# Kernel optimization log

Measured on AMD Instinct MI355X. Metric: run time of the kernel, lower is better.

The kernel has to match this reference:

```python
import jax, jax.numpy as jnp
import numpy as np

SOFT_CAP = 20.0
NEG_BIG = -1e9


def setup_inputs() -> dict:
    key = jax.random.key(0)
    kq, kk, kv = jax.random.split(key, 3)
    T, H, D = 3072, 16, 128
    lens = np.array([1024, 768, 640, 640], dtype=np.int32)  # sums to T, max 1024
    cu = np.concatenate([[0], np.cumsum(lens)]).astype(np.int32)
    q = jax.random.normal(kq, (T, H, D), dtype=jnp.float32)
    k = jax.random.normal(kk, (T, H, D), dtype=jnp.float32)
    v = jax.random.normal(kv, (T, H, D), dtype=jnp.float32)
    return {
        "q": q, "k": k, "v": v,
        "cu_seqlens_q": jnp.asarray(cu), "cu_seqlens_k": jnp.asarray(cu),
        "max_seqlen_q": 1024, "max_seqlen_k": 1024,
    }


def _varlen_attention(q, k, v, cu_q, cu_k, S_q, S_k):
    # q,k,v: [T, H, D] packed; cu_*: [B+1] prefix sums; S_*: static max seqlens
    T, H, D = q.shape
    B = cu_q.shape[0] - 1
    lens_q = cu_q[1:] - cu_q[:-1]  # [B]
    lens_k = cu_k[1:] - cu_k[:-1]
    ar_q = jnp.arange(S_q)
    ar_k = jnp.arange(S_k)
    # pad packed tokens into [B, S, H, D]
    idx_q = jnp.clip(cu_q[:-1, None] + ar_q[None, :], 0, T - 1)  # [B, S_q]
    idx_k = jnp.clip(cu_k[:-1, None] + ar_k[None, :], 0, k.shape[0] - 1)
    mask_k = ar_k[None, :] < lens_k[:, None]  # [B, S_k] valid keys
    qp = q[idx_q]  # [B, S_q, H, D]
    kp = k[idx_k]  # [B, S_k, H, D]
    vp = v[idx_k]
    scale = 1.0 / jnp.sqrt(jnp.float32(D))
    scores = jnp.einsum("bqhd,bkhd->bhqk", qp, kp) * scale  # [B, H, S_q, S_k] fp32
    scores = jnp.tanh(scores / SOFT_CAP) * SOFT_CAP  # logit soft-cap
    scores = jnp.where(mask_k[:, None, None, :], scores, NEG_BIG)
    w = jax.nn.softmax(scores, axis=-1)
    out = jnp.einsum("bhqk,bkhd->bqhd", w, vp)  # [B, S_q, H, D]
    # unpad back to packed [T, H, D]
    t = jnp.arange(T)
    seg = jnp.searchsorted(cu_q, t, side="right") - 1  # sequence id per token
    pos = seg * S_q + (t - cu_q[seg])
    return out.reshape(B * S_q, H, D)[pos]


def reference(q, k, v, cu_seqlens_q, cu_seqlens_k, max_seqlen_q, max_seqlen_k):
    return _varlen_attention(q, k, v, cu_seqlens_q, cu_seqlens_k,
                             int(max_seqlen_q), int(max_seqlen_k))
```

## Files before the change

### kernel.cpp

```cpp
#include <hip/hip_runtime.h>

#define H_ 16
#define D_ 128

typedef __attribute__((ext_vector_type(4))) float f32x4;
typedef __attribute__((ext_vector_type(8))) short bf8_t;
typedef __attribute__((ext_vector_type(4))) unsigned int u32x4;

__device__ __forceinline__ unsigned cvt_pk(float a, float b) {
  unsigned r;
  asm("v_cvt_pk_bf16_f32 %0, %1, %2" : "=v"(r) : "v"(a), "v"(b));
  return r;
}

__device__ __forceinline__ float exp2a(float x) {
  float r;
  asm("v_exp_f32 %0, %1" : "=v"(r) : "v"(x));
  return r;
}

__device__ __forceinline__ bf8_t cvt8(const f32x4 a, const f32x4 b) {
  u32x4 r;
  r[0] = cvt_pk(a[0], a[1]); r[1] = cvt_pk(a[2], a[3]);
  r[2] = cvt_pk(b[0], b[1]); r[3] = cvt_pk(b[2], b[3]);
  return __builtin_bit_cast(bf8_t, r);
}

__global__ __launch_bounds__(128)
void conv_kv(const float* __restrict__ K, const float* __restrict__ V,
             const int* __restrict__ cuk, short* __restrict__ Kbf,
             short* __restrict__ Vt, int B, int T) {
  const int J0 = blockIdx.x * 8;
  const int h  = blockIdx.y;
  int b = 0;
  while (b + 1 < B && J0 >= cuk[b + 1]) ++b;
  const int k0 = cuk[b];

  {
    const int g = J0 + (threadIdx.x >> 4);
    const int c = threadIdx.x & 15;
    const int sub = c ^ ((g - k0) & 7);
    const float* src = K + ((size_t)g * H_ + h) * D_ + sub * 8;
    *(bf8_t*)(Kbf + ((size_t)g * H_ + h) * D_ + c * 8) =
        cvt8(*(const f32x4*)src, *(const f32x4*)(src + 4));
  }
  {
    const int d  = threadIdx.x;
    const int j0 = J0 - k0;
    const int base = k0 + (j0 >> 6) * 64 + 32 * ((j0 >> 5) & 1) + 4 * ((j0 >> 3) & 3);
    float v[8];
    #pragma unroll
    for (int s = 0; s < 8; ++s)
      v[s] = V[((size_t)(base + 16 * (s >> 2) + (s & 3)) * H_ + h) * D_ + d];
    u32x4 w;
    w[0] = cvt_pk(v[0], v[1]); w[1] = cvt_pk(v[2], v[3]);
    w[2] = cvt_pk(v[4], v[5]); w[3] = cvt_pk(v[6], v[7]);
    *(u32x4*)(Vt + ((size_t)h * D_ + d) * T + J0) = w;
  }
}

__global__ __launch_bounds__(256, 2)
void fa_main(const float* __restrict__ Q, const short* __restrict__ Kbf,
             const short* __restrict__ Vt, const int* __restrict__ cuq,
             const int* __restrict__ cuk, float* __restrict__ O, int B, int T) {
  __shared__ __align__(16) short k_lds[2][64 * 128];
  __shared__ __align__(16) short v_lds[2][64 * 128];

  const int slot = blockIdx.x;
  int bmax = 0, nmax = 0, tot = 0;
  for (int bb = 0; bb < B; ++bb) {
    const int nk = (cuk[bb + 1] - cuk[bb] + 63) >> 6;
    if (nk > nmax) { nmax = nk; bmax = bb; }
    tot += ((cuq[bb + 1] - cuq[bb] + 127) >> 7) * 16;
  }
  if (slot >= tot) return;
  const int L = ((cuq[bmax + 1] - cuq[bmax] + 127) >> 7) * 16;
  const int halfS = (tot - L) >> 1;

  int b = -1, item = 0;
  if (slot >= halfS && slot < halfS + L) {
    b = bmax; item = slot - halfS;
  } else {
    int sidx = (slot < halfS) ? slot : slot - L;
    for (int bb = 0; bb < B; ++bb) {
      if (bb == bmax) continue;
      const int it = ((cuq[bb + 1] - cuq[bb] + 127) >> 7) * 16;
      if (sidx < it) { b = bb; item = sidx; break; }
      sidx -= it;
    }
    if (b < 0) return;
  }
  const int qt = item >> 4;
  const int h  = item & 15;

  const int q0   = cuq[b];
  const int lenq = cuq[b + 1] - q0;
  const int k0   = cuk[b];
  const int lenk = cuk[b + 1] - k0;
  const int nkt  = (lenk + 63) >> 6;

  const int tid  = threadIdx.x;
  const int wave = tid >> 6;
  const int lane = tid & 63;
  const int lo   = lane & 15;
  const int gp   = lane >> 4;

  const int qrow_base = qt * 128 + wave * 32;

  bf8_t qf[2][4];
  #pragma unroll
  for (int s2 = 0; s2 < 2; ++s2) {
    const int qr = qrow_base + s2 * 16 + lo;
    const int qg = q0 + (qr < lenq ? qr : lenq - 1);
    const float* qp = Q + ((size_t)qg * H_ + h) * D_;
    #pragma unroll
    for (int db = 0; db < 4; ++db) {
      const f32x4 a = *reinterpret_cast<const f32x4*>(qp + db * 32 + gp * 8);
      const f32x4 c = *reinterpret_cast<const f32x4*>(qp + db * 32 + gp * 8 + 4);
      qf[s2][db] = cvt8(a, c);
    }
  }

  f32x4 acc[2][8];
  #pragma unroll
  for (int s2 = 0; s2 < 2; ++s2)
    #pragma unroll
    for (int i = 0; i < 8; ++i) acc[s2][i] = f32x4{0.f, 0.f, 0.f, 0.f};
  f32x4 acc_l[2] = {f32x4{0.f, 0.f, 0.f, 0.f}, f32x4{0.f, 0.f, 0.f, 0.f}};

  bf8_t onesf;
  #pragma unroll
  for (int i = 0; i < 8; ++i) onesf[i] = (short)0x3F80;

  const int skey = tid >> 4;
  const int ssub = tid & 15;
  const int vd5  = tid >> 3;
  const int vcp  = tid & 7;
  const int vclog = vcp ^ (vd5 & 7);
  const short* KbH = Kbf + h * D_ + ssub * 8;
  const short* VtH = Vt + ((size_t)h * D_) * T;

  const float cy  = 0.12752749f;
  const float ce  = 28.853901f;
  const float ycl = 19.620652f;
  const float c3p = -4.0037686e-4f;
  const float c4p = 1.9236228e-7f;

  u32x4 krb[4], vrb[4];
  auto issue_loads = [&](int kb) {
    #pragma unroll
    for (int i = 0; i < 4; ++i) {
      const int kk = kb + skey + 16 * i;
      const size_t gk = (size_t)(k0 + (kk < lenk ? kk : lenk - 1));
      krb[i] = *(const u32x4*)(KbH + gk * (H_ * D_));
    }
    #pragma unroll
    for (int i = 0; i < 4; ++i) {
      const int d = i * 32 + vd5;
      vrb[i] = *(const u32x4*)(VtH + (size_t)d * T + (k0 + kb + vclog * 8));
    }
  };
  auto write_tile = [&](int buf) {
    char* kb2 = (char*)k_lds[buf];
    char* vb2 = (char*)v_lds[buf];
    #pragma unroll
    for (int i = 0; i < 4; ++i)
      *(u32x4*)(kb2 + (skey + 16 * i) * 256 + ssub * 16) = krb[i];
    #pragma unroll
    for (int i = 0; i < 4; ++i)
      *(u32x4*)(vb2 + (i * 32 + vd5) * 128 + vcp * 16) = vrb[i];
  };

  issue_loads(0);
  write_tile(0);
  __syncthreads();

  for (int kt = 0; kt < nkt; ++kt) {
    const int kb = kt * 64;
    char* kbase = (char*)k_lds[kt & 1];
    char* vtb   = (char*)v_lds[kt & 1];

    if (kt + 1 < nkt) issue_loads(kb + 64);
    __builtin_amdgcn_sched_barrier(0);

    f32x4 s[2][4];
    #pragma unroll
    for (int s2 = 0; s2 < 2; ++s2)
      #pragma unroll
      for (int kq = 0; kq < 4; ++kq) s[s2][kq] = f32x4{0.f, 0.f, 0.f, 0.f};
    __builtin_amdgcn_s_setprio(1);
    #pragma unroll
    for (int db = 0; db < 4; ++db) {
      #pragma unroll
      for (int kq = 0; kq < 4; ++kq) {
        const bf8_t kf = *(const bf8_t*)(kbase + (kq * 16 + lo) * 256 +
                                         (((4 * db + gp) ^ (lo & 7)) << 4));
        s[0][kq] = __builtin_amdgcn_mfma_f32_16x16x32_bf16(kf, qf[0][db], s[0][kq], 0, 0, 0);
        s[1][kq] = __builtin_amdgcn_mfma_f32_16x16x32_bf16(kf, qf[1][db], s[1][kq], 0, 0, 0);
      }
    }
    __builtin_amdgcn_s_setprio(0);

    const bool fullTile = (kb + 64 <= lenk);
    if (fullTile) {
      #pragma unroll
      for (int s2 = 0; s2 < 2; ++s2) {
        #pragma unroll
        for (int kq = 0; kq < 4; ++kq) {
          #pragma unroll
          for (int r = 0; r < 4; ++r) {
            float y = s[s2][kq][r] * cy;
            y = __builtin_amdgcn_fmed3f(y, -ycl, ycl);
            const float u = y * y;
            const float pol = fmaf(u, fmaf(u, c4p, c3p), 1.0f);
            s[s2][kq][r] = exp2a(fmaf(y, pol, -ce));
          }
        }
      }
    } else {
      #pragma unroll
      for (int s2 = 0; s2 < 2; ++s2) {
        #pragma unroll
        for (int kq = 0; kq < 4; ++kq) {
          const int keyb = kb + 16 * kq + 4 * gp;
          #pragma unroll
          for (int r = 0; r < 4; ++r) {
            float y = s[s2][kq][r] * cy;
            y = __builtin_amdgcn_fmed3f(y, -ycl, ycl);
            const float u = y * y;
            const float pol = fmaf(u, fmaf(u, c4p, c3p), 1.0f);
            float p = exp2a(fmaf(y, pol, -ce));
            s[s2][kq][r] = (keyb + r < lenk) ? p : 0.0f;
          }
        }
      }
    }

    u32x4 pf[2][2];
    #pragma unroll
    for (int s2 = 0; s2 < 2; ++s2) {
      #pragma unroll
      for (int ks = 0; ks < 2; ++ks) {
        pf[s2][ks][0] = cvt_pk(s[s2][2 * ks][0], s[s2][2 * ks][1]);
        pf[s2][ks][1] = cvt_pk(s[s2][2 * ks][2], s[s2][2 * ks][3]);
        pf[s2][ks][2] = cvt_pk(s[s2][2 * ks + 1][0], s[s2][2 * ks + 1][1]);
        pf[s2][ks][3] = cvt_pk(s[s2][2 * ks + 1][2], s[s2][2 * ks + 1][3]);
      }
    }

    if (kt + 1 < nkt) write_tile((kt + 1) & 1);

    __builtin_amdgcn_s_setprio(1);
    #pragma unroll
    for (int ks = 0; ks < 2; ++ks) {
      acc_l[0] = __builtin_amdgcn_mfma_f32_16x16x32_bf16(
          __builtin_bit_cast(bf8_t, pf[0][ks]), onesf, acc_l[0], 0, 0, 0);
      acc_l[1] = __builtin_amdgcn_mfma_f32_16x16x32_bf16(
          __builtin_bit_cast(bf8_t, pf[1][ks]), onesf, acc_l[1], 0, 0, 0);
      #pragma unroll
      for (int nt = 0; nt < 8; ++nt) {
        const int d = nt * 16 + lo;
        const bf8_t vf = *(const bf8_t*)(
            vtb + d * 128 + ((((ks << 2) + gp) ^ (lo & 7)) << 4));
        acc[0][nt] = __builtin_amdgcn_mfma_f32_16x16x32_bf16(
            __builtin_bit_cast(bf8_t, pf[0][ks]), vf, acc[0][nt], 0, 0, 0);
        acc[1][nt] = __builtin_amdgcn_mfma_f32_16x16x32_bf16(
            __builtin_bit_cast(bf8_t, pf[1][ks]), vf, acc[1][nt], 0, 0, 0);
      }
    }
    __builtin_amdgcn_s_setprio(0);

    __syncthreads();
  }

  #pragma unroll
  for (int s2 = 0; s2 < 2; ++s2) {
    #pragma unroll
    for (int r = 0; r < 4; ++r) {
      const float inv_l = 1.0f / acc_l[s2][r];
      const int qr = qrow_base + s2 * 16 + 4 * gp + r;
      if (qr < lenq) {
        float* op = O + ((size_t)(q0 + qr) * H_ + h) * D_;
        #pragma unroll
        for (int nt = 0; nt < 8; ++nt)
          op[nt * 16 + lo] = acc[s2][nt][r] * inv_l;
      }
    }
  }
}

extern "C" void kernel_launch(void* const* d_in, const int* in_sizes, int n_in,
                              void* d_out, int out_size, void* d_ws, size_t ws_size,
                              hipStream_t stream) {
  const float* Q  = (const float*)d_in[0];
  const float* K  = (const float*)d_in[1];
  const float* V  = (const float*)d_in[2];
  const int* cuq  = (const int*)d_in[3];
  const int* cuk  = (const int*)d_in[4];
  float* out      = (float*)d_out;
  const int B = in_sizes[3] - 1;
  const int T = in_sizes[0] / (H_ * D_);

  short* Kbf = (short*)d_ws;
  short* Vt  = Kbf + (size_t)T * H_ * D_;

  conv_kv<<<dim3(T / 8, H_), 128, 0, stream>>>(K, V, cuk, Kbf, Vt, B, T);
  const int maxItems = 16 * (T / 128 + B);
  fa_main<<<maxItems, 256, 0, stream>>>(Q, Kbf, Vt, cuq, cuk, out, B, T);
}
```

Baseline: 61.54 us.

## Switch to single-buffered 128-key tiles with a post-compute LDS write

Doubles the key tile from 64 to 128 keys and drops the LDS double buffer for one 128-key buffer per K and V. Global loads for the next tile are still issued early into registers, but the LDS write now happens after compute behind an extra barrier. The aim is to halve loop iterations and barrier count per key, at the cost of doubled register staging (krb/vrb at 8 entries) and less overlap between LDS writes and MFMA work. The register pressure risks spills or lower occupancy under launch_bounds(256,2).

```diff
diff --git a/kernel.cpp b/kernel.cpp
--- a/kernel.cpp
+++ b/kernel.cpp
@@ -63,8 +63,8 @@
 void fa_main(const float* __restrict__ Q, const short* __restrict__ Kbf,
              const short* __restrict__ Vt, const int* __restrict__ cuq,
              const int* __restrict__ cuk, float* __restrict__ O, int B, int T) {
-  __shared__ __align__(16) short k_lds[2][64 * 128];
-  __shared__ __align__(16) short v_lds[2][64 * 128];
+  __shared__ __align__(16) short k_lds[128 * 128];
+  __shared__ __align__(16) short v_lds[128 * 128];
 
   const int slot = blockIdx.x;
   int bmax = 0, nmax = 0, tot = 0;
@@ -97,7 +97,7 @@
   const int lenq = cuq[b + 1] - q0;
   const int k0   = cuk[b];
   const int lenk = cuk[b + 1] - k0;
-  const int nkt  = (lenk + 63) >> 6;
+  const int nkt2 = (lenk + 127) >> 7;
 
   const int tid  = threadIdx.x;
   const int wave = tid >> 6;
@@ -146,122 +146,127 @@
   const float c3p = -4.0037686e-4f;
   const float c4p = 1.9236228e-7f;
 
-  u32x4 krb[4], vrb[4];
+  u32x4 krb[8], vrb[8];
   auto issue_loads = [&](int kb) {
     #pragma unroll
-    for (int i = 0; i < 4; ++i) {
+    for (int i = 0; i < 8; ++i) {
       const int kk = kb + skey + 16 * i;
       const size_t gk = (size_t)(k0 + (kk < lenk ? kk : lenk - 1));
       krb[i] = *(const u32x4*)(KbH + gk * (H_ * D_));
     }
     #pragma unroll
-    for (int i = 0; i < 4; ++i) {
-      const int d = i * 32 + vd5;
-      vrb[i] = *(const u32x4*)(VtH + (size_t)d * T + (k0 + kb + vclog * 8));
+    for (int i = 0; i < 8; ++i) {
+      const int half = i >> 2;
+      const int d = (i & 3) * 32 + vd5;
+      vrb[i] = *(const u32x4*)(VtH + (size_t)d * T + (k0 + kb + half * 64 + vclog * 8));
     }
   };
-  auto write_tile = [&](int buf) {
-    char* kb2 = (char*)k_lds[buf];
-    char* vb2 = (char*)v_lds[buf];
-    #pragma unroll
-    for (int i = 0; i < 4; ++i)
+  auto write_tile = [&]() {
+    char* kb2 = (char*)k_lds;
+    char* vb2 = (char*)v_lds;
+    #pragma unroll
+    for (int i = 0; i < 8; ++i)
       *(u32x4*)(kb2 + (skey + 16 * i) * 256 + ssub * 16) = krb[i];
     #pragma unroll
-    for (int i = 0; i < 4; ++i)
-      *(u32x4*)(vb2 + (i * 32 + vd5) * 128 + vcp * 16) = vrb[i];
+    for (int i = 0; i < 8; ++i) {
+      const int half = i >> 2;
+      const int d = (i & 3) * 32 + vd5;
+      *(u32x4*)(vb2 + d * 256 + (half * 8 + vcp) * 16) = vrb[i];
+    }
   };
 
   issue_loads(0);
-  write_tile(0);
+  write_tile();
   __syncthreads();
 
-  for (int kt = 0; kt < nkt; ++kt) {
-    const int kb = kt * 64;
-    char* kbase = (char*)k_lds[kt & 1];
-    char* vtb   = (char*)v_lds[kt & 1];
-
-    if (kt + 1 < nkt) issue_loads(kb + 64);
+  for (int kt = 0; kt < nkt2; ++kt) {
+    const int kb = kt * 128;
+
+    if (kt + 1 < nkt2) issue_loads(kb + 128);
     __builtin_amdgcn_sched_barrier(0);
 
-    f32x4 s[2][4];
-    #pragma unroll
-    for (int s2 = 0; s2 < 2; ++s2)
+    const bool fullTile = (kb + 128 <= lenk);
+    u32x4 pf[2][4];
+
+    #pragma unroll
+    for (int half = 0; half < 2; ++half) {
+      f32x4 s[2][4];
       #pragma unroll
-      for (int kq = 0; kq < 4; ++kq) s[s2][kq] = f32x4{0.f, 0.f, 0.f, 0.f};
-    __builtin_amdgcn_s_setprio(1);
-    #pragma unroll
-    for (int db = 0; db < 4; ++db) {
+      for (int s2 = 0; s2 < 2; ++s2)
+        #pragma unroll
+        for (int kq = 0; kq < 4; ++kq) s[s2][kq] = f32x4{0.f, 0.f, 0.f, 0.f};
+      __builtin_amdgcn_s_setprio(1);
       #pragma unroll
-      for (int kq = 0; kq < 4; ++kq) {
-        const bf8_t kf = *(const bf8_t*)(kbase + (kq * 16 + lo) * 256 +
-                                         (((4 * db + gp) ^ (lo & 7)) << 4));
-        s[0][kq] = __builtin_amdgcn_mfma_f32_16x16x32_bf16(kf, qf[0][db], s[0][kq], 0, 0, 0);
-        s[1][kq] = __builtin_amdgcn_mfma_f32_16x16x32_bf16(kf, qf[1][db], s[1][kq], 0, 0, 0);
-      }
-    }
-    __builtin_amdgcn_s_setprio(0);
-
-    const bool fullTile = (kb + 64 <= lenk);
-    if (fullTile) {
+      for (int db = 0; db < 4; ++db) {
+        #pragma unroll
+        for (int kq = 0; kq < 4; ++kq) {
+          const bf8_t kf = *(const bf8_t*)((char*)k_lds +
+              (half * 64 + kq * 16 + lo) * 256 + (((4 * db + gp) ^ (lo & 7)) << 4));
+          s[0][kq] = __builtin_amdgcn_mfma_f32_16x16x32_bf16(kf, qf[0][db], s[0][kq], 0, 0, 0);
+          s[1][kq] = __builtin_amdgcn_mfma_f32_16x16x32_bf16(kf, qf[1][db], s[1][kq], 0, 0, 0);
+        }
+      }
+      __builtin_amdgcn_s_setprio(0);
+
+      if (fullTile) {
+        #pragma unroll
+        for (int s2 = 0; s2 < 2; ++s2) {
+          #pragma unroll
+          for (int kq = 0; kq < 4; ++kq) {
+            #pragma unroll
+            for (int r = 0; r < 4; ++r) {
+              float y = s[s2][kq][r] * cy;
+              y = __builtin_amdgcn_fmed3f(y, -ycl, ycl);
+              const float u = y * y;
+              const float pol = fmaf(u, fmaf(u, c4p, c3p), 1.0f);
+              s[s2][kq][r] = exp2a(fmaf(y, pol, -ce));
+            }
+          }
+        }
+      } else {
+        #pragma unroll
+        for (int s2 = 0; s2 < 2; ++s2) {
+          #pragma unroll
+          for (int kq = 0; kq < 4; ++kq) {
+            const int keyb = kb + half * 64 + 16 * kq + 4 * gp;
+            #pragma unroll
+            for (int r = 0; r < 4; ++r) {
+              float y = s[s2][kq][r] * cy;
+              y = __builtin_amdgcn_fmed3f(y, -ycl, ycl);
+              const float u = y * y;
+              const float pol = fmaf(u, fmaf(u, c4p, c3p), 1.0f);
+              float p = exp2a(fmaf(y, pol, -ce));
+              s[s2][kq][r] = (keyb + r < lenk) ? p : 0.0f;
+            }
+          }
+        }
+      }
+
       #pragma unroll
       for (int s2 = 0; s2 < 2; ++s2) {
         #pragma unroll
-        for (int kq = 0; kq < 4; ++kq) {
-          #pragma unroll
-          for (int r = 0; r < 4; ++r) {
-            float y = s[s2][kq][r] * cy;
-            y = __builtin_amdgcn_fmed3f(y, -ycl, ycl);
-            const float u = y * y;
-            const float pol = fmaf(u, fmaf(u, c4p, c3p), 1.0f);
-            s[s2][kq][r] = exp2a(fmaf(y, pol, -ce));
-          }
+        for (int ksl = 0; ksl < 2; ++ksl) {
+          pf[s2][half * 2 + ksl][0] = cvt_pk(s[s2][2 * ksl][0], s[s2][2 * ksl][1]);
+          pf[s2][half * 2 + ksl][1] = cvt_pk(s[s2][2 * ksl][2], s[s2][2 * ksl][3]);
+          pf[s2][half * 2 + ksl][2] = cvt_pk(s[s2][2 * ksl + 1][0], s[s2][2 * ksl + 1][1]);
+          pf[s2][half * 2 + ksl][3] = cvt_pk(s[s2][2 * ksl + 1][2], s[s2][2 * ksl + 1][3]);
         }
       }
-    } else {
-      #pragma unroll
-      for (int s2 = 0; s2 < 2; ++s2) {
-        #pragma unroll
-        for (int kq = 0; kq < 4; ++kq) {
-          const int keyb = kb + 16 * kq + 4 * gp;
-          #pragma unroll
-          for (int r = 0; r < 4; ++r) {
-            float y = s[s2][kq][r] * cy;
-            y = __builtin_amdgcn_fmed3f(y, -ycl, ycl);
-            const float u = y * y;
-            const float pol = fmaf(u, fmaf(u, c4p, c3p), 1.0f);
-            float p = exp2a(fmaf(y, pol, -ce));
-            s[s2][kq][r] = (keyb + r < lenk) ? p : 0.0f;
-          }
-        }
-      }
-    }
-
-    u32x4 pf[2][2];
-    #pragma unroll
-    for (int s2 = 0; s2 < 2; ++s2) {
-      #pragma unroll
-      for (int ks = 0; ks < 2; ++ks) {
-        pf[s2][ks][0] = cvt_pk(s[s2][2 * ks][0], s[s2][2 * ks][1]);
-        pf[s2][ks][1] = cvt_pk(s[s2][2 * ks][2], s[s2][2 * ks][3]);
-        pf[s2][ks][2] = cvt_pk(s[s2][2 * ks + 1][0], s[s2][2 * ks + 1][1]);
-        pf[s2][ks][3] = cvt_pk(s[s2][2 * ks + 1][2], s[s2][2 * ks + 1][3]);
-      }
-    }
-
-    if (kt + 1 < nkt) write_tile((kt + 1) & 1);
+    }
 
     __builtin_amdgcn_s_setprio(1);
     #pragma unroll
-    for (int ks = 0; ks < 2; ++ks) {
+    for (int ks = 0; ks < 4; ++ks) {
       acc_l[0] = __builtin_amdgcn_mfma_f32_16x16x32_bf16(
           __builtin_bit_cast(bf8_t, pf[0][ks]), onesf, acc_l[0], 0, 0, 0);
       acc_l[1] = __builtin_amdgcn_mfma_f32_16x16x32_bf16(
           __builtin_bit_cast(bf8_t, pf[1][ks]), onesf, acc_l[1], 0, 0, 0);
+      const int half = ks >> 1;
       #pragma unroll
       for (int nt = 0; nt < 8; ++nt) {
         const int d = nt * 16 + lo;
-        const bf8_t vf = *(const bf8_t*)(
-            vtb + d * 128 + ((((ks << 2) + gp) ^ (lo & 7)) << 4));
+        const bf8_t vf = *(const bf8_t*)((char*)v_lds + d * 256 +
+            ((half * 8 + ((((ks & 1) << 2) + gp) ^ (lo & 7))) << 4));
         acc[0][nt] = __builtin_amdgcn_mfma_f32_16x16x32_bf16(
             __builtin_bit_cast(bf8_t, pf[0][ks]), vf, acc[0][nt], 0, 0, 0);
         acc[1][nt] = __builtin_amdgcn_mfma_f32_16x16x32_bf16(
@@ -271,6 +276,10 @@
     __builtin_amdgcn_s_setprio(0);
 
     __syncthreads();
+    if (kt + 1 < nkt2) {
+      write_tile();
+      __syncthreads();
+    }
   }
 
   #pragma unroll
```

After: 78.69 us. 27.9% more time.
